# Kernel optimization log

Hardware: AMD Instinct MI355X
Metric: run time of the kernel (lower is better)

## Reference

```python
import jax, jax.numpy as jnp
import numpy as np

DIM = 1024        # model dim
HEADS = 1         # num_heads (fc1 in_features==1 forces this)
HDIM = DIM // HEADS
INNER = 16        # dim_inner
B, L = 2, 4096
ROPE_BASE = 32.0


def _apply_rope(x, pos, base):
    # x: [b, l, h, d]; standard rotate-half RoPE
    d = x.shape[-1]
    inv_freq = base ** (-jnp.arange(0, d, 2, dtype=jnp.float32) / d)   # [d/2]
    ang = pos[:, None].astype(jnp.float32) * inv_freq                  # [l, d/2]
    emb = jnp.concatenate([ang, ang], axis=-1)                         # [l, d]
    cos = jnp.cos(emb)[None, :, None, :].astype(x.dtype)
    sin = jnp.sin(emb)[None, :, None, :].astype(x.dtype)
    x1, x2 = x[..., : d // 2], x[..., d // 2:]
    rot = jnp.concatenate([-x2, x1], axis=-1)
    return x * cos + rot * sin


def setup_inputs() -> dict:
    key = jax.random.key(0)
    ks = jax.random.split(key, 7)
    hidden_states = jax.random.normal(ks[0], (B, L, DIM), dtype=jnp.float32)
    Wq = jax.random.normal(ks[1], (DIM, DIM), dtype=jnp.float32) * 0.02
    Wk = jax.random.normal(ks[2], (DIM, DIM), dtype=jnp.float32) * 0.02
    fc1_w = jax.random.normal(ks[3], (INNER, 1), dtype=jnp.float32) * 0.1
    fc1_b = jax.random.normal(ks[4], (INNER,), dtype=jnp.float32) * 0.1
    fc2_w = jax.random.normal(ks[5], (DIM, INNER), dtype=jnp.float32) * 0.1
    fc2_b = jax.random.normal(ks[6], (DIM,), dtype=jnp.float32) * 0.1
    return {"hidden_states": hidden_states, "Wq": Wq, "Wk": Wk,
            "fc1_w": fc1_w, "fc1_b": fc1_b, "fc2_w": fc2_w, "fc2_b": fc2_b}


def reference(hidden_states, Wq, Wk, fc1_w, fc1_b, fc2_w, fc2_b):
    b, l, _ = hidden_states.shape
    # projections, cast to bf16 as in the torch module
    q = (hidden_states @ Wq.T).reshape(b, l, HEADS, HDIM).astype(jnp.bfloat16)
    k = (hidden_states @ Wk.T).reshape(b, l, HEADS, HDIM).astype(jnp.bfloat16)
    pos = jnp.arange(l)
    q = _apply_rope(q, pos, ROPE_BASE)
    k = _apply_rope(k, pos, ROPE_BASE)
    # causal exp(QK) with NO softmax normalization; accumulate in fp32
    scores = jnp.einsum('bqhd,bkhd->bhqk',
                        q.astype(jnp.float32), k.astype(jnp.float32)) / (HDIM ** 0.5)
    causal = jnp.tril(jnp.ones((l, l), dtype=bool))                    # [l, l]
    exp_qk = jnp.where(causal[None, None], jnp.exp(scores), 0.0)       # [b, h, l, l]
    o = jnp.swapaxes(exp_qk.sum(axis=-1), 1, 2)                        # [b, l, h]
    # small MLP: h(=1) -> INNER -> DIM
    o = jax.nn.relu(o @ fc1_w.T + fc1_b)
    return o @ fc2_w.T + fc2_b                                         # [b, l, DIM]
```

## Files before the change

kernel.cpp:

```cpp
#include <hip/hip_runtime.h>
#include <hip/hip_bf16.h>

typedef __bf16 bf16_t;
typedef __bf16 bf16x4 __attribute__((ext_vector_type(4)));
typedef __bf16 bf16x8 __attribute__((ext_vector_type(8)));
typedef float f32x4 __attribute__((ext_vector_type(4)));

#define B_   2
#define L_   4096
#define DIM_ 1024
#define M_   (B_ * L_)
#define NTASK2_ 272

__device__ __forceinline__ void ld_g2l_16(const bf16_t* g, bf16_t* l) {
  __builtin_amdgcn_global_load_lds(
      (__attribute__((address_space(1))) void*)g,
      (__attribute__((address_space(3))) void*)l, 16, 0, 0);
}

__global__ void cvt_all(const float* __restrict__ hs, const float* __restrict__ wq,
                        const float* __restrict__ wk, bf16_t* __restrict__ hs_b,
                        bf16_t* __restrict__ wq_b, bf16_t* __restrict__ wk_b,
                        float* __restrict__ o) {
  const int N_HS = M_ * DIM_ / 4, N_W = DIM_ * DIM_ / 4;
  int i = blockIdx.x * blockDim.x + threadIdx.x;
  if (i < M_ / 4) ((float4*)o)[i] = float4{0.f, 0.f, 0.f, 0.f};
  const float* s; bf16_t* d; int idx;
  if (i < N_HS)            { s = hs; d = hs_b; idx = i; }
  else if (i < N_HS + N_W) { s = wq; d = wq_b; idx = i - N_HS; }
  else                     { s = wk; d = wk_b; idx = i - N_HS - N_W; }
  float4 v = ((const float4*)s)[idx];
  bf16x4 ov = { (bf16_t)v.x, (bf16_t)v.y, (bf16_t)v.z, (bf16_t)v.w };
  ((bf16x4*)d)[idx] = ov;
}

template <bool PAIRK>
__device__ __forceinline__ void core256(const bf16_t* __restrict__ A,
                                        const bf16_t* __restrict__ B0,
                                        const bf16_t* __restrict__ B1,
                                        bf16_t* sm, bool active,
                                        f32x4 (&acc)[4][4]) {
  constexpr int BUF = 24 * 512;
  const int tid  = threadIdx.x;
  const int wave = tid >> 6, lane = tid & 63;
  const int wm = wave >> 1, wn = wave & 1;
  const int quad = lane >> 4, l16 = lane & 15;
  const int srow = lane >> 2;
  const int scol = (((lane & 3) ^ ((lane >> 3) & 3)) * 8);
  const int rsw  = ((l16 >> 1) & 3) * 8;
  const int loff = l16 * 32 + ((quad * 8) ^ rsw);

  const bf16_t* gA0 = A + (size_t)(wave * 16 + srow) * DIM_ + scol;
  const bf16_t* gA1 = A + (size_t)((wave + 8) * 16 + srow) * DIM_ + scol;
  const bf16_t* gB  = (wave < 4)
      ? B0 + (size_t)(wave * 16 + srow) * DIM_ + scol
      : B1 + (size_t)((wave - 4) * 16 + srow) * DIM_ + scol;

  bf16_t* p0 = sm;
  bf16_t* p1 = sm + BUF;
  bf16_t* p2 = sm + 2 * BUF;

  auto stage = [&](int kk, bf16_t* buf) {
    ld_g2l_16(gA0 + kk, buf + wave * 512);
    ld_g2l_16(gA1 + kk, buf + (wave + 8) * 512);
    ld_g2l_16(gB + kk, buf + (16 + wave) * 512);
  };

  stage(0, p0);
  stage(32, p1);
  asm volatile("s_waitcnt vmcnt(3)" ::: "memory");
  __builtin_amdgcn_s_barrier();

  for (int s = 0; s < 32; ++s) {
    bf16x8 aF[4], bF[4];
    if (active) {
#pragma unroll
      for (int rf = 0; rf < 4; ++rf)
        aF[rf] = *(const bf16x8*)(p0 + (wm * 4 + rf) * 512 + loff);
#pragma unroll
      for (int cf = 0; cf < 4; ++cf) {
        int k = PAIRK ? ((cf & 1) + wn * 2 + (cf >> 1) * 4)
                      : ((cf & 3) + wn * 4);
        bF[cf] = *(const bf16x8*)(p0 + (16 + k) * 512 + loff);
      }
    }
    if (s < 30) stage((s + 2) * 32, p2);
    __builtin_amdgcn_s_barrier();
    asm volatile("s_waitcnt lgkmcnt(0)" ::: "memory");
    __builtin_amdgcn_sched_barrier(0);
    if (active) {
      __builtin_amdgcn_s_setprio(1);
#pragma unroll
      for (int rf = 0; rf < 4; ++rf)
#pragma unroll
        for (int cf = 0; cf < 4; ++cf)
          acc[rf][cf] = __builtin_amdgcn_mfma_f32_16x16x32_bf16(
              aF[rf], bF[cf], acc[rf][cf], 0, 0, 0);
      __builtin_amdgcn_s_setprio(0);
    }
    if (s < 30)       asm volatile("s_waitcnt vmcnt(3)" ::: "memory");
    else if (s == 30) asm volatile("s_waitcnt vmcnt(0)" ::: "memory");
    __builtin_amdgcn_s_barrier();
    bf16_t* t0 = p0; p0 = p1; p1 = p2; p2 = t0;
  }
}

__global__ __launch_bounds__(512, 4)
void proj_gemm(const bf16_t* __restrict__ A, const bf16_t* __restrict__ Wqb,
               const bf16_t* __restrict__ Wkb, bf16_t* __restrict__ Cq,
               bf16_t* __restrict__ Ck) {
  __shared__ __attribute__((aligned(16))) bf16_t sm[3 * 24 * 512];
  const int bid = blockIdx.x;
  const int xcd = bid & 7, slot = bid >> 3;
  const int m0 = (xcd * 4 + (slot >> 4)) * 256;
  const int zn = slot & 15;
  const int z = zn >> 3, n0 = (zn & 7) * 64;
  const bf16_t* Wb = z ? Wkb : Wqb;
  bf16_t* Cm = z ? Ck : Cq;

  f32x4 acc[4][4] = {};
  core256<true>(A + (size_t)m0 * DIM_, Wb + (size_t)n0 * DIM_,
                Wb + (size_t)(n0 + 512) * DIM_, sm, true, acc);

  const int tid = threadIdx.x, wave = tid >> 6, lane = tid & 63;
  const int wm = wave >> 1, wn = wave & 1;
  const int quad = lane >> 4, l16 = lane & 15;

  float inv[2];
#pragma unroll
  for (int c2 = 0; c2 < 2; ++c2) {
    int j = n0 + (c2 + wn * 2) * 16 + l16;
    inv[c2] = exp2f((float)j * (-5.0f / 512.0f));
  }
#pragma unroll
  for (int rf = 0; rf < 4; ++rf)
#pragma unroll
    for (int r = 0; r < 4; ++r) {
      int m = m0 + wm * 64 + rf * 16 + quad * 4 + r;
      float posf = (float)(m & (L_ - 1));
#pragma unroll
      for (int c2 = 0; c2 < 2; ++c2) {
        int j = n0 + (c2 + wn * 2) * 16 + l16;
        float ang = posf * inv[c2];
        float c = cosf(ang), s = sinf(ang);
        float cb = (float)(bf16_t)c, sb = (float)(bf16_t)s;
        float x1 = (float)(bf16_t)acc[rf][c2][r];
        float x2 = (float)(bf16_t)acc[rf][c2 + 2][r];
        Cm[(size_t)m * DIM_ + j]       = (bf16_t)(x1 * cb - x2 * sb);
        Cm[(size_t)m * DIM_ + j + 512] = (bf16_t)(x2 * cb + x1 * sb);
      }
    }
}

__global__ __launch_bounds__(512, 4)
void attn_rowsum(const bf16_t* __restrict__ Q, const bf16_t* __restrict__ Kc,
                 float* __restrict__ o) {
  __shared__ __attribute__((aligned(16))) bf16_t sm[3 * 24 * 512];
  int logical = (blockIdx.x & 7) * 68 + (blockIdx.x >> 3);
  int b = logical / NTASK2_;
  int t = logical - b * NTASK2_;
  int mi = (int)((sqrtf(4.0f * (float)t + 1.0f) - 1.0f) * 0.5f);
  while ((mi + 1) * (mi + 2) <= t) ++mi;
  while (mi * (mi + 1) > t) --mi;
  int nt = t - mi * (mi + 1);

  const int tid = threadIdx.x, wave = tid >> 6, lane = tid & 63;
  const int wm = wave >> 1, wn = wave & 1;
  const int quad = lane >> 4, l16 = lane & 15;

  const bf16_t* A  = Q  + (size_t)b * L_ * DIM_ + (size_t)mi * 256 * DIM_;
  const bf16_t* Bp = Kc + (size_t)b * L_ * DIM_ + (size_t)nt * 128 * DIM_;

  bool active = (mi * 256 + wm * 64 + 63) >= nt * 128;

  f32x4 acc[4][4] = {};
  core256<false>(A, Bp, Bp + (size_t)64 * DIM_, sm, active, acc);

  if (active) {
    const bool masked = (nt >= 2 * mi);
#pragma unroll
    for (int rf = 0; rf < 4; ++rf) {
#pragma unroll
      for (int r = 0; r < 4; ++r) {
        int grow = mi * 256 + wm * 64 + rf * 16 + quad * 4 + r;
        float sum = 0.0f;
#pragma unroll
        for (int cf = 0; cf < 4; ++cf) {
          int gcol = nt * 128 + wn * 64 + cf * 16 + l16;
          float e = __expf(acc[rf][cf][r] * 0.03125f);
          if (!masked || gcol <= grow) sum += e;
        }
        sum += __shfl_xor(sum, 1);
        sum += __shfl_xor(sum, 2);
        sum += __shfl_xor(sum, 4);
        sum += __shfl_xor(sum, 8);
        if (l16 == 0)
          atomicAdd(&o[b * L_ + grow], sum);
      }
    }
  }
}

__global__ __launch_bounds__(256)
void mlp_out_kernel(const float* __restrict__ o, const float* __restrict__ fc1_w,
                    const float* __restrict__ fc1_b, const float* __restrict__ fc2_w,
                    const float* __restrict__ fc2_b, float* __restrict__ out) {
  const int R = 16;
  int row0 = blockIdx.x * R;
  int tid = threadIdx.x;
  __shared__ float h[R][16];
  {
    int rl = tid >> 4, i = tid & 15;
    float s = o[row0 + rl];
    h[rl][i] = fmaxf(fc1_w[i] * s + fc1_b[i], 0.0f);
  }
  __syncthreads();
  int d = tid * 4;
  float w[4][16];
#pragma unroll
  for (int c = 0; c < 4; ++c)
#pragma unroll
    for (int i = 0; i < 16; ++i) w[c][i] = fc2_w[(d + c) * 16 + i];
  float4 bb = *(const float4*)(fc2_b + d);
  for (int rl = 0; rl < R; ++rl) {
    float4 v = bb;
#pragma unroll
    for (int i = 0; i < 16; ++i) {
      float hv = h[rl][i];
      v.x += w[0][i] * hv; v.y += w[1][i] * hv;
      v.z += w[2][i] * hv; v.w += w[3][i] * hv;
    }
    *(float4*)(out + (size_t)(row0 + rl) * DIM_ + d) = v;
  }
}

extern "C" void kernel_launch(void* const* d_in, const int* in_sizes, int n_in,
                              void* d_out, int out_size, void* d_ws, size_t ws_size,
                              hipStream_t stream) {
  const float* hs    = (const float*)d_in[0];
  const float* Wq    = (const float*)d_in[1];
  const float* Wk    = (const float*)d_in[2];
  const float* fc1_w = (const float*)d_in[3];
  const float* fc1_b = (const float*)d_in[4];
  const float* fc2_w = (const float*)d_in[5];
  const float* fc2_b = (const float*)d_in[6];
  float* out = (float*)d_out;

  char* ws = (char*)d_ws;
  bf16_t* hs_bf = (bf16_t*)ws; ws += (size_t)M_ * DIM_ * 2;
  bf16_t* wq_bf = (bf16_t*)ws; ws += (size_t)DIM_ * DIM_ * 2;
  bf16_t* wk_bf = (bf16_t*)ws; ws += (size_t)DIM_ * DIM_ * 2;
  bf16_t* q_bf  = (bf16_t*)ws; ws += (size_t)M_ * DIM_ * 2;
  bf16_t* k_bf  = (bf16_t*)ws; ws += (size_t)M_ * DIM_ * 2;
  float*  o     = (float*)ws;

  const int n4 = (M_ * DIM_ + 2 * DIM_ * DIM_) / 4;
  cvt_all<<<n4 / 256, 256, 0, stream>>>(hs, Wq, Wk, hs_bf, wq_bf, wk_bf, o);

  proj_gemm<<<512, 512, 0, stream>>>(hs_bf, wq_bf, wk_bf, q_bf, k_bf);

  attn_rowsum<<<544, 512, 0, stream>>>(q_bf, k_bf, o);

  mlp_out_kernel<<<M_ / 16, 256, 0, stream>>>(o, fc1_w, fc1_b, fc2_w, fc2_b, out);
}
```

Baseline: 236.2 us.

## Stage projection epilogue through LDS for coalesced stores; grid-stride conversion, nontemporal outputs

The projection GEMM epilogue now writes RoPE'd results into shared memory and then emits 16-byte coalesced nontemporal stores, instead of scattered 2-byte global writes. The conversion kernel switches to a fixed 2048-block grid-stride loop. The MLP output uses nontemporal float4 stores. These target write-coalescing and cache pollution at the cost of extra barriers and an LDS round trip. Zeroing of o still only covers i0 < M/4, and 2048*256 threads is enough for that.

```diff
diff --git a/kernel.cpp b/kernel.cpp
--- a/kernel.cpp
+++ b/kernel.cpp
@@ -23,15 +23,18 @@
                         bf16_t* __restrict__ wq_b, bf16_t* __restrict__ wk_b,
                         float* __restrict__ o) {
   const int N_HS = M_ * DIM_ / 4, N_W = DIM_ * DIM_ / 4;
-  int i = blockIdx.x * blockDim.x + threadIdx.x;
-  if (i < M_ / 4) ((float4*)o)[i] = float4{0.f, 0.f, 0.f, 0.f};
-  const float* s; bf16_t* d; int idx;
-  if (i < N_HS)            { s = hs; d = hs_b; idx = i; }
-  else if (i < N_HS + N_W) { s = wq; d = wq_b; idx = i - N_HS; }
-  else                     { s = wk; d = wk_b; idx = i - N_HS - N_W; }
-  float4 v = ((const float4*)s)[idx];
-  bf16x4 ov = { (bf16_t)v.x, (bf16_t)v.y, (bf16_t)v.z, (bf16_t)v.w };
-  ((bf16x4*)d)[idx] = ov;
+  const int NT = N_HS + 2 * N_W;
+  int i0 = blockIdx.x * blockDim.x + threadIdx.x;
+  if (i0 < M_ / 4) ((float4*)o)[i0] = float4{0.f, 0.f, 0.f, 0.f};
+  for (int i = i0; i < NT; i += gridDim.x * blockDim.x) {
+    const float* s; bf16_t* d; int idx;
+    if (i < N_HS)            { s = hs; d = hs_b; idx = i; }
+    else if (i < N_HS + N_W) { s = wq; d = wq_b; idx = i - N_HS; }
+    else                     { s = wk; d = wk_b; idx = i - N_HS - N_W; }
+    float4 v = ((const float4*)s)[idx];
+    bf16x4 ov = { (bf16_t)v.x, (bf16_t)v.y, (bf16_t)v.z, (bf16_t)v.w };
+    ((bf16x4*)d)[idx] = ov;
+  }
 }
 
 template <bool PAIRK>
@@ -132,24 +135,38 @@
     int j = n0 + (c2 + wn * 2) * 16 + l16;
     inv[c2] = exp2f((float)j * (-5.0f / 512.0f));
   }
+
+  __syncthreads();
 #pragma unroll
   for (int rf = 0; rf < 4; ++rf)
 #pragma unroll
     for (int r = 0; r < 4; ++r) {
-      int m = m0 + wm * 64 + rf * 16 + quad * 4 + r;
-      float posf = (float)(m & (L_ - 1));
+      int row = wm * 64 + rf * 16 + quad * 4 + r;
+      float posf = (float)((m0 + row) & (L_ - 1));
 #pragma unroll
       for (int c2 = 0; c2 < 2; ++c2) {
-        int j = n0 + (c2 + wn * 2) * 16 + l16;
+        int jl = (c2 + wn * 2) * 16 + l16;
         float ang = posf * inv[c2];
         float c = cosf(ang), s = sinf(ang);
         float cb = (float)(bf16_t)c, sb = (float)(bf16_t)s;
         float x1 = (float)(bf16_t)acc[rf][c2][r];
         float x2 = (float)(bf16_t)acc[rf][c2 + 2][r];
-        Cm[(size_t)m * DIM_ + j]       = (bf16_t)(x1 * cb - x2 * sb);
-        Cm[(size_t)m * DIM_ + j + 512] = (bf16_t)(x2 * cb + x1 * sb);
+        sm[row * 136 + jl]      = (bf16_t)(x1 * cb - x2 * sb);
+        sm[row * 136 + 64 + jl] = (bf16_t)(x2 * cb + x1 * sb);
       }
     }
+  __syncthreads();
+#pragma unroll
+  for (int it = 0; it < 8; ++it) {
+    int idx = it * 512 + tid;
+    int row = idx >> 4;
+    int ch  = idx & 15;
+    int g   = ch >> 3;
+    int c8  = (ch & 7) * 8;
+    bf16x8 v = *(const bf16x8*)(sm + row * 136 + g * 64 + c8);
+    __builtin_nontemporal_store(
+        v, (bf16x8*)(Cm + (size_t)(m0 + row) * DIM_ + n0 + (size_t)g * 512 + c8));
+  }
 }
 
 __global__ __launch_bounds__(512, 4)
@@ -230,7 +247,9 @@
       v.x += w[0][i] * hv; v.y += w[1][i] * hv;
       v.z += w[2][i] * hv; v.w += w[3][i] * hv;
     }
-    *(float4*)(out + (size_t)(row0 + rl) * DIM_ + d) = v;
+    f32x4 vv = { v.x, v.y, v.z, v.w };
+    __builtin_nontemporal_store(
+        vv, (f32x4*)(out + (size_t)(row0 + rl) * DIM_ + d));
   }
 }
 
@@ -254,8 +273,7 @@
   bf16_t* k_bf  = (bf16_t*)ws; ws += (size_t)M_ * DIM_ * 2;
   float*  o     = (float*)ws;
 
-  const int n4 = (M_ * DIM_ + 2 * DIM_ * DIM_) / 4;
-  cvt_all<<<n4 / 256, 256, 0, stream>>>(hs, Wq, Wk, hs_bf, wq_bf, wk_bf, o);
+  cvt_all<<<2048, 256, 0, stream>>>(hs, Wq, Wk, hs_bf, wq_bf, wk_bf, o);
 
   proj_gemm<<<512, 512, 0, stream>>>(hs_bf, wq_bf, wk_bf, q_bf, k_bf);
 
```

After: 237.9 us. Within noise of the previous version (+0.7%).
